# Kernel optimization log

Hardware: AMD Instinct MI355X
Metric: run time of the kernel (lower is better)

The kernel has to match this reference:

```python
import jax, jax.numpy as jnp
import numpy as np

N_GRAPHS = 256      # graphs in the batch
N_PER = 52          # nodes per peptide graph (module default num_nodes=52)
IN_CH = 21          # amino-acid one-hot features
HIDDEN = 128
OUT_EG = 128
LATENT = 64
N_LAYERS = 4


def _fc_edges(n_graphs, n_per):
    """Block-diagonal fully-connected directed edges (no self loops)."""
    base = np.arange(n_per)
    r, c = np.meshgrid(base, base, indexing='ij')
    mask = r != c
    r, c = r[mask], c[mask]                       # [n_per*(n_per-1)]
    offs = (np.arange(n_graphs) * n_per)[:, None]
    row = (r[None, :] + offs).reshape(-1)
    col = (c[None, :] + offs).reshape(-1)
    return row.astype(np.int32), col.astype(np.int32)


def setup_inputs() -> dict:
    key = jax.random.key(0)
    ks = iter(jax.random.split(key, 40))

    def rn(shape, scale=0.05):
        return jax.random.normal(next(ks), shape, dtype=jnp.float32) * scale

    N = N_GRAPHS * N_PER
    row, col = _fc_edges(N_GRAPHS, N_PER)
    L, H = N_LAYERS, HIDDEN
    return {
        'x': jax.random.normal(next(ks), (N, IN_CH), dtype=jnp.float32),
        'pos': jax.random.normal(next(ks), (N, 3), dtype=jnp.float32),
        'edge_row': jnp.asarray(row),
        'edge_col': jnp.asarray(col),
        'batch': jnp.repeat(jnp.arange(N_GRAPHS, dtype=jnp.int32), N_PER),
        'emb_in_w': rn((IN_CH, H)), 'emb_in_b': jnp.zeros((H,), jnp.float32),
        'edge_w1': rn((L, 2 * H + 1, H)), 'edge_b1': jnp.zeros((L, H), jnp.float32),
        'edge_w2': rn((L, H, H)), 'edge_b2': jnp.zeros((L, H), jnp.float32),
        'node_w1': rn((L, 2 * H, H)), 'node_b1': jnp.zeros((L, H), jnp.float32),
        'node_w2': rn((L, H, H)), 'node_b2': jnp.zeros((L, H), jnp.float32),
        'coord_w1': rn((L, H, H)), 'coord_b1': jnp.zeros((L, H), jnp.float32),
        'coord_w2': rn((L, H, 1), scale=0.001),   # xavier gain=0.001, no bias
        'emb_out_w': rn((H, OUT_EG)), 'emb_out_b': jnp.zeros((OUT_EG,), jnp.float32),
        'mean_w': rn((OUT_EG, LATENT)), 'mean_b': jnp.zeros((LATENT,), jnp.float32),
        'logvar_w': rn((OUT_EG, LATENT)), 'logvar_b': jnp.zeros((LATENT,), jnp.float32),
    }


def _segment_mean(data, ids, n):
    s = jax.ops.segment_sum(data, ids, num_segments=n)
    cnt = jax.ops.segment_sum(jnp.ones((data.shape[0],), data.dtype), ids, num_segments=n)
    return s / jnp.clip(cnt, 1.0)[:, None]


def _egcl(h, coord, row, col, p):
    """One E_GCL layer (residual=True, coords_agg='mean', no attention/tanh/normalize)."""
    ew1, eb1, ew2, eb2, nw1, nb1, nw2, nb2, cw1, cb1, cw2 = p
    n = h.shape[0]
    coord_diff = coord[row] - coord[col]                     # [E,3]
    radial = jnp.sum(coord_diff * coord_diff, axis=1, keepdims=True)  # [E,1]
    # edge model
    m = jnp.concatenate([h[row], h[col], radial], axis=1)    # [E,2H+1]
    m = jax.nn.silu(m @ ew1 + eb1)
    edge_feat = jax.nn.silu(m @ ew2 + eb2)                   # [E,H]
    # coord model: per-edge scalar, mean-aggregated onto source nodes
    t = jax.nn.silu(edge_feat @ cw1 + cb1) @ cw2             # [E,1]
    coord = coord + _segment_mean(coord_diff * t, row, n)
    # node model: sum-aggregate edge features, MLP, residual
    agg = jax.ops.segment_sum(edge_feat, row, num_segments=n)
    z = jnp.concatenate([h, agg], axis=1)                    # [N,2H]
    z = jax.nn.silu(z @ nw1 + nb1)
    h = h + (z @ nw2 + nb2)
    return h, coord


def reference(x, pos, edge_row, edge_col, batch,
              emb_in_w, emb_in_b,
              edge_w1, edge_b1, edge_w2, edge_b2,
              node_w1, node_b1, node_w2, node_b2,
              coord_w1, coord_b1, coord_w2,
              emb_out_w, emb_out_b,
              mean_w, mean_b, logvar_w, logvar_b):
    h = x @ emb_in_w + emb_in_b
    coord = pos
    for i in range(edge_w1.shape[0]):
        h, coord = _egcl(h, coord, edge_row, edge_col,
                         (edge_w1[i], edge_b1[i], edge_w2[i], edge_b2[i],
                          node_w1[i], node_b1[i], node_w2[i], node_b2[i],
                          coord_w1[i], coord_b1[i], coord_w2[i]))
    h = h @ emb_out_w + emb_out_b                            # embedding_out
    g = _segment_mean(h, batch, N_GRAPHS)                    # global_mean_pool
    mean = g @ mean_w + mean_b
    log_var = g @ logvar_w + logvar_b
    return mean, log_var
```

## Files before the change

kernel.cpp:

```cpp
#include <hip/hip_runtime.h>

constexpr int NPER = 52;
constexpr int HID  = 128;
constexpr int INCH = 21;
constexpr int NLAY = 4;
constexpr int LATD = 64;
constexpr int NGRAPH = 256;
constexpr int TPB  = 1024;
constexpr int TSTR = 424;
constexpr int TILE = 16 * TSTR;

typedef short short8 __attribute__((ext_vector_type(8)));
typedef float f32x4  __attribute__((ext_vector_type(4)));

constexpr int W1T_OFF = 0;
constexpr int W1T_SZ  = NLAY * 256 * HID;
constexpr int W2T_OFF = W1T_OFF + W1T_SZ;
constexpr int W2T_SZ  = NLAY * HID * HID;
constexpr int C1T_OFF = W2T_OFF + W2T_SZ;
constexpr int C1T_SZ  = NLAY * HID * HID;
constexpr int N1T_OFF = C1T_OFF + C1T_SZ;
constexpr int N1T_SZ  = NLAY * HID * 2 * HID;
constexpr int N2T_OFF = N1T_OFF + N1T_SZ;
constexpr int N2T_SZ  = NLAY * HID * HID;
constexpr int WS_ELEMS = N2T_OFF + N2T_SZ;

__device__ __forceinline__ unsigned cvt_pk_bf16(float a, float b) {
    unsigned r;
    asm("v_cvt_pk_bf16_f32 %0, %1, %2" : "=v"(r) : "v"(a), "v"(b));
    return r;
}
__device__ __forceinline__ unsigned short f2bf(float f) {
    return (unsigned short)cvt_pk_bf16(f, f);
}
__device__ __forceinline__ float bf2f(unsigned short h) {
    return __uint_as_float(((unsigned)h) << 16);
}
__device__ __forceinline__ float fast_rcp(float x) {
    float r;
    asm("v_rcp_f32 %0, %1" : "=v"(r) : "v"(x));
    return r;
}
__device__ __forceinline__ float silu_f(float v) {
    return v * fast_rcp(1.0f + __expf(-v));
}
__device__ __forceinline__ f32x4 mfma16(short8 a, short8 b, f32x4 c) {
    return __builtin_amdgcn_mfma_f32_16x16x32_bf16(a, b, c, 0, 0, 0);
}

__device__ __forceinline__ int tidx(int row, int e) {
    return (e >> 3) * TSTR + row * 8 + (e & 7);
}

__global__ void conv_w(const float* __restrict__ ew1, const float* __restrict__ ew2,
                       const float* __restrict__ cw1, const float* __restrict__ nw1,
                       const float* __restrict__ nw2, unsigned short* __restrict__ ws)
{
    int idx = blockIdx.x * 256 + threadIdx.x;
    if (idx >= WS_ELEMS) return;
    float v;
    if (idx < W2T_OFF) {
        int t = idx - W1T_OFF;
        int L = t / (256 * HID), rem = t % (256 * HID);
        int n = rem / HID, k = rem % HID;
        v = (n < HID) ? ew1[(size_t)L * 257 * HID + k * HID + n]
                      : ew1[(size_t)L * 257 * HID + (HID + k) * HID + (n - HID)];
    } else if (idx < C1T_OFF) {
        int t = idx - W2T_OFF;
        int L = t / (HID * HID), rem = t % (HID * HID);
        int n = rem / HID, k = rem % HID;
        v = ew2[(size_t)L * HID * HID + k * HID + n];
    } else if (idx < N1T_OFF) {
        int t = idx - C1T_OFF;
        int L = t / (HID * HID), rem = t % (HID * HID);
        int n = rem / HID, k = rem % HID;
        v = cw1[(size_t)L * HID * HID + k * HID + n];
    } else if (idx < N2T_OFF) {
        int t = idx - N1T_OFF;
        int L = t / (HID * 2 * HID), rem = t % (HID * 2 * HID);
        int n = rem / (2 * HID), k = rem % (2 * HID);
        v = nw1[(size_t)L * 2 * HID * HID + k * HID + n];
    } else {
        int t = idx - N2T_OFF;
        int L = t / (HID * HID), rem = t % (HID * HID);
        int n = rem / HID, k = rem % HID;
        v = nw2[(size_t)L * HID * HID + k * HID + n];
    }
    ws[idx] = f2bf(v);
}

constexpr int LDS_FLOATS = 1024 + 156 + 156 + 128 + 512 + 128;
constexpr size_t SHMEM_BYTES = (size_t)8 * TILE * 2 + LDS_FLOATS * 4;

__device__ __forceinline__ void coord_agg(int r, int rr, const float* tpart,
                                          const float* coord_s, float* cacc_s, int lane)
{
    float dx = 0.f, dy = 0.f, dz = 0.f;
    if (lane < NPER) {
        const float* tb = tpart + rr * 256;
        float tc = tb[lane] + tb[64 + lane] + tb[128 + lane] + tb[192 + lane];
        dx = (coord_s[r * 3 + 0] - coord_s[lane * 3 + 0]) * tc;
        dy = (coord_s[r * 3 + 1] - coord_s[lane * 3 + 1]) * tc;
        dz = (coord_s[r * 3 + 2] - coord_s[lane * 3 + 2]) * tc;
    }
    #pragma unroll
    for (int m = 1; m < 64; m <<= 1) {
        dx += __shfl_xor(dx, m); dy += __shfl_xor(dy, m); dz += __shfl_xor(dz, m);
    }
    if (lane == 0) {
        cacc_s[r * 3 + 0] = dx; cacc_s[r * 3 + 1] = dy; cacc_s[r * 3 + 2] = dz;
    }
}

extern "C" __global__ void __launch_bounds__(TPB)
egnn_mfma(const float* __restrict__ x, const float* __restrict__ pos,
          const float* __restrict__ emb_in_w, const float* __restrict__ emb_in_b,
          const float* __restrict__ edge_w1,
          const float* __restrict__ edge_b1, const float* __restrict__ edge_b2,
          const float* __restrict__ node_b1, const float* __restrict__ node_b2,
          const float* __restrict__ coord_b1, const float* __restrict__ coord_w2,
          const float* __restrict__ emb_out_w, const float* __restrict__ emb_out_b,
          const float* __restrict__ mean_w, const float* __restrict__ mean_b,
          const float* __restrict__ logvar_w, const float* __restrict__ logvar_b,
          const unsigned short* __restrict__ ws, float* __restrict__ out)
{
    extern __shared__ __align__(16) char smem[];
    unsigned short* m0_t = (unsigned short*)smem;
    unsigned short* m1_t = m0_t + TILE;
    unsigned short* e0_t = m1_t + TILE;
    unsigned short* e1_t = e0_t + TILE;
    unsigned short* h_t  = e1_t + TILE;
    unsigned short* ag_t = h_t  + TILE;
    unsigned short* A_t  = ag_t + TILE;
    unsigned short* B_t  = A_t  + TILE;
    float* aggp    = (float*)(B_t + TILE);
    float* coord_s = aggp + 1024;
    float* cacc_s  = coord_s + 156;
    float* rad_s   = cacc_s + 156;
    float* tpart   = rad_s + 128;
    float* wr_s    = tpart + 512;

    const int g    = blockIdx.x;
    const int tid  = threadIdx.x;
    const int lane = tid & 63;
    const int wv   = tid >> 6;
    const int mp   = wv >> 2;
    const int np   = wv & 3;
    const int l15  = lane & 15;
    const int kb   = lane >> 4;
    const int rowA = mp * 16 + l15;
    const int crow0 = mp * 16 + kb * 4;
    const int n0   = 32 * np + l15;
    const int n1   = n0 + 16;
    const int jp   = 2 * lane;
    const int pb   = (jp >> 3) * TSTR + (jp & 7);
    const int fo   = kb * TSTR + rowA * 8;

    {
        float* xs = (float*)m0_t;
        for (int p = tid; p < NPER * INCH; p += TPB) xs[p] = x[(size_t)g * NPER * INCH + p];
        for (int p = tid; p < NPER * 3; p += TPB)    coord_s[p] = pos[(size_t)g * NPER * 3 + p];
    }
    __syncthreads();

    for (int p = tid; p < NPER * HID; p += TPB) {
        int c = p >> 7, j = p & 127;
        float s = emb_in_b[j];
        #pragma unroll 7
        for (int k = 0; k < INCH; ++k) s += ((float*)m0_t)[c * INCH + k] * emb_in_w[k * HID + j];
        h_t[tidx(c, j)] = f2bf(s);
    }
    __syncthreads();

    for (int L = 0; L < NLAY; ++L) {
        const unsigned short* w1t = ws + W1T_OFF + (size_t)L * 256 * HID;
        const unsigned short* w2t = ws + W2T_OFF + (size_t)L * HID * HID;
        const unsigned short* c1t = ws + C1T_OFF + (size_t)L * HID * HID;
        const unsigned short* n1t = ws + N1T_OFF + (size_t)L * HID * 2 * HID;
        const unsigned short* n2t = ws + N2T_OFF + (size_t)L * HID * HID;

        short8 wE[8], wC[8];
        #pragma unroll
        for (int s = 0; s < 4; ++s) {
            wE[s]     = *(const short8*)(w2t + (size_t)n0 * HID + 32 * s + 8 * kb);
            wE[4 + s] = *(const short8*)(w2t + (size_t)n1 * HID + 32 * s + 8 * kb);
            wC[s]     = *(const short8*)(c1t + (size_t)n0 * HID + 32 * s + 8 * kb);
            wC[4 + s] = *(const short8*)(c1t + (size_t)n1 * HID + 32 * s + 8 * kb);
        }
        float eb2v[2], cb1v[2], cw2v[2];
        eb2v[0] = edge_b2[L * HID + n0];  eb2v[1] = edge_b2[L * HID + n1];
        cb1v[0] = coord_b1[L * HID + n0]; cb1v[1] = coord_b1[L * HID + n1];
        cw2v[0] = coord_w2[L * HID + n0]; cw2v[1] = coord_w2[L * HID + n1];
        if (tid < HID) wr_s[tid] = edge_w1[(size_t)L * 257 * HID + 256 * HID + tid];

        {
            f32x4 acc[4];
            #pragma unroll
            for (int q = 0; q < 4; ++q) acc[q] = (f32x4){0.f, 0.f, 0.f, 0.f};
            #pragma unroll
            for (int s = 0; s < 4; ++s) {
                short8 af = *(const short8*)(h_t + fo + s * 4 * TSTR);
                #pragma unroll
                for (int q = 0; q < 4; ++q) {
                    int n = l15 + 16 * (4 * np + q);
                    short8 bf = *(const short8*)(w1t + (size_t)n * HID + 32 * s + 8 * kb);
                    acc[q] = mfma16(af, bf, acc[q]);
                }
            }
            #pragma unroll
            for (int q = 0; q < 4; ++q) {
                int n = l15 + 16 * (4 * np + q);
                float eb1 = (n < HID) ? edge_b1[L * HID + n] : 0.f;
                #pragma unroll
                for (int reg = 0; reg < 4; ++reg) {
                    int c = crow0 + reg;
                    if (c < NPER) {
                        float v = acc[q][reg] + eb1;
                        if (n < HID) A_t[tidx(c, n)] = f2bf(v);
                        else         B_t[tidx(c, n - HID)] = f2bf(v);
                    }
                }
            }
        }
        if (tid < NPER) {
            float dx = coord_s[0] - coord_s[tid * 3 + 0];
            float dy = coord_s[1] - coord_s[tid * 3 + 1];
            float dz = coord_s[2] - coord_s[tid * 3 + 2];
            rad_s[tid] = dx * dx + dy * dy + dz * dz;
        } else if (tid >= 64 && tid < 64 + NPER) {
            int c = tid - 64;
            float dx = coord_s[3] - coord_s[c * 3 + 0];
            float dy = coord_s[4] - coord_s[c * 3 + 1];
            float dz = coord_s[5] - coord_s[c * 3 + 2];
            rad_s[64 + c] = dx * dx + dy * dy + dz * dz;
        }
        __syncthreads();

        const float wrl = wr_s[jp], wrh = wr_s[jp + 1];

        for (int gp = 0; gp < 26; ++gp) {
            const int r0 = 2 * gp, r1 = r0 + 1;

            {
                unsigned pa0 = *(const unsigned*)(A_t + pb + r0 * 8);
                unsigned pa1 = *(const unsigned*)(A_t + pb + r1 * 8);
                float A0l = bf2f((unsigned short)(pa0 & 0xffff)), A0h = bf2f((unsigned short)(pa0 >> 16));
                float A1l = bf2f((unsigned short)(pa1 & 0xffff)), A1h = bf2f((unsigned short)(pa1 >> 16));
                for (int j = wv; j < 2 * NPER; j += 16) {
                    int rr = (j >= NPER);
                    int c  = rr ? j - NPER : j;
                    float Al = rr ? A1l : A0l, Ah = rr ? A1h : A0h;
                    float rad = rad_s[rr * 64 + c];
                    unsigned bp = *(const unsigned*)(B_t + pb + c * 8);
                    float v0 = Al + bf2f((unsigned short)(bp & 0xffff)) + rad * wrl;
                    float v1 = Ah + bf2f((unsigned short)(bp >> 16))    + rad * wrh;
                    unsigned mv = cvt_pk_bf16(silu_f(v0), silu_f(v1));
                    *(unsigned*)((rr ? m1_t : m0_t) + pb + c * 8) = mv;
                }
            }
            __syncthreads();

            {
                f32x4 e00 = (f32x4){0.f,0.f,0.f,0.f}, e01 = e00, e10 = e00, e11 = e00;
                #pragma unroll
                for (int s = 0; s < 4; ++s) {
                    short8 af0 = *(const short8*)(m0_t + fo + s * 4 * TSTR);
                    short8 af1 = *(const short8*)(m1_t + fo + s * 4 * TSTR);
                    e00 = mfma16(af0, wE[s], e00); e01 = mfma16(af0, wE[4 + s], e01);
                    e10 = mfma16(af1, wE[s], e10); e11 = mfma16(af1, wE[4 + s], e11);
                }
                #pragma unroll
                for (int rr = 0; rr < 2; ++rr) {
                    f32x4 ea = rr ? e10 : e00, eb = rr ? e11 : e01;
                    unsigned short* et = rr ? e1_t : e0_t;
                    const int r = rr ? r1 : r0;
                    float a0 = 0.f, a1 = 0.f;
                    #pragma unroll
                    for (int reg = 0; reg < 4; ++reg) {
                        int c = crow0 + reg;
                        float v0 = silu_f(ea[reg] + eb2v[0]);
                        float v1 = silu_f(eb[reg] + eb2v[1]);
                        if (c < NPER) {
                            et[tidx(c, n0)] = f2bf(v0);
                            et[tidx(c, n1)] = f2bf(v1);
                            if (c != r) { a0 += v0; a1 += v1; }
                        }
                    }
                    a0 += __shfl_xor(a0, 16); a0 += __shfl_xor(a0, 32);
                    a1 += __shfl_xor(a1, 16); a1 += __shfl_xor(a1, 32);
                    if (kb == 0) {
                        float* ar = aggp + (rr * 4 + mp) * HID;
                        ar[n0] = a0; ar[n1] = a1;
                    }
                }
                if (wv < 2 && gp > 0) coord_agg(2 * gp - 2 + wv, wv, tpart, coord_s, cacc_s, lane);
            }
            __syncthreads();

            {
                f32x4 y00 = (f32x4){0.f,0.f,0.f,0.f}, y01 = y00, y10 = y00, y11 = y00;
                #pragma unroll
                for (int s = 0; s < 4; ++s) {
                    short8 af0 = *(const short8*)(e0_t + fo + s * 4 * TSTR);
                    short8 af1 = *(const short8*)(e1_t + fo + s * 4 * TSTR);
                    y00 = mfma16(af0, wC[s], y00); y01 = mfma16(af0, wC[4 + s], y01);
                    y10 = mfma16(af1, wC[s], y10); y11 = mfma16(af1, wC[4 + s], y11);
                }
                #pragma unroll
                for (int rr = 0; rr < 2; ++rr) {
                    f32x4 ya = rr ? y10 : y00, yb = rr ? y11 : y01;
                    float* tp = tpart + (rr * 4 + np) * 64;
                    #pragma unroll
                    for (int reg = 0; reg < 4; ++reg) {
                        float v = silu_f(ya[reg] + cb1v[0]) * cw2v[0]
                                + silu_f(yb[reg] + cb1v[1]) * cw2v[1];
                        v += __shfl_xor(v, 1); v += __shfl_xor(v, 2);
                        v += __shfl_xor(v, 4); v += __shfl_xor(v, 8);
                        if (l15 == 0) tp[crow0 + reg] = v;
                    }
                }
            }
            if (tid < 256) {
                int rr = tid >> 7, t = tid & 127;
                const float* ap = aggp + rr * 512;
                float a = ap[t] + ap[128 + t] + ap[256 + t] + ap[384 + t];
                ag_t[tidx(2 * gp + rr, t)] = f2bf(a);
            } else if (tid < 384 && gp + 1 < 26) {
                int t = tid - 256, rr = t >> 6, c = t & 63;
                if (c < NPER) {
                    int r = 2 * (gp + 1) + rr;
                    float dx = coord_s[r * 3 + 0] - coord_s[c * 3 + 0];
                    float dy = coord_s[r * 3 + 1] - coord_s[c * 3 + 1];
                    float dz = coord_s[r * 3 + 2] - coord_s[c * 3 + 2];
                    rad_s[rr * 64 + c] = dx * dx + dy * dy + dz * dz;
                }
            }
            __syncthreads();
        }

        if (wv < 2) coord_agg(50 + wv, wv, tpart, coord_s, cacc_s, lane);
        {
            float nb1v[2];
            nb1v[0] = node_b1[L * HID + n0]; nb1v[1] = node_b1[L * HID + n1];
            f32x4 z0 = (f32x4){0.f,0.f,0.f,0.f}, z1 = z0;
            #pragma unroll
            for (int s = 0; s < 4; ++s) {
                short8 af = *(const short8*)(h_t + fo + s * 4 * TSTR);
                z0 = mfma16(af, *(const short8*)(n1t + (size_t)n0 * 2 * HID + 32 * s + 8 * kb), z0);
                z1 = mfma16(af, *(const short8*)(n1t + (size_t)n1 * 2 * HID + 32 * s + 8 * kb), z1);
            }
            #pragma unroll
            for (int s = 0; s < 4; ++s) {
                short8 af = *(const short8*)(ag_t + fo + s * 4 * TSTR);
                z0 = mfma16(af, *(const short8*)(n1t + (size_t)n0 * 2 * HID + HID + 32 * s + 8 * kb), z0);
                z1 = mfma16(af, *(const short8*)(n1t + (size_t)n1 * 2 * HID + HID + 32 * s + 8 * kb), z1);
            }
            #pragma unroll
            for (int reg = 0; reg < 4; ++reg) {
                int c = crow0 + reg;
                if (c < NPER) {
                    m0_t[tidx(c, n0)] = f2bf(silu_f(z0[reg] + nb1v[0]));
                    m0_t[tidx(c, n1)] = f2bf(silu_f(z1[reg] + nb1v[1]));
                }
            }
        }
        __syncthreads();

        if (tid < NPER * 3) coord_s[tid] += cacc_s[tid] * (1.0f / 51.0f);
        {
            float nb2v[2];
            nb2v[0] = node_b2[L * HID + n0]; nb2v[1] = node_b2[L * HID + n1];
            f32x4 d0 = (f32x4){0.f,0.f,0.f,0.f}, d1 = d0;
            #pragma unroll
            for (int s = 0; s < 4; ++s) {
                short8 af = *(const short8*)(m0_t + fo + s * 4 * TSTR);
                d0 = mfma16(af, *(const short8*)(n2t + (size_t)n0 * HID + 32 * s + 8 * kb), d0);
                d1 = mfma16(af, *(const short8*)(n2t + (size_t)n1 * HID + 32 * s + 8 * kb), d1);
            }
            #pragma unroll
            for (int reg = 0; reg < 4; ++reg) {
                int c = crow0 + reg;
                if (c < NPER) {
                    int i0 = tidx(c, n0), i1 = tidx(c, n1);
                    h_t[i0] = f2bf(bf2f(h_t[i0]) + d0[reg] + nb2v[0]);
                    h_t[i1] = f2bf(bf2f(h_t[i1]) + d1[reg] + nb2v[1]);
                }
            }
        }
        __syncthreads();
    }

    float* gm = aggp;
    float* eg = aggp + HID;
    if (tid < HID) {
        float s = 0.f;
        for (int c = 0; c < NPER; ++c) s += bf2f(h_t[tidx(c, tid)]);
        gm[tid] = s * (1.0f / 52.0f);
    }
    __syncthreads();
    if (tid < HID) {
        float s = emb_out_b[tid];
        #pragma unroll 4
        for (int k = 0; k < HID; ++k) s += gm[k] * emb_out_w[k * HID + tid];
        eg[tid] = s;
    }
    __syncthreads();
    if (tid < 2 * LATD) {
        const int  l   = tid & (LATD - 1);
        const bool ism = tid < LATD;
        const float* W = ism ? mean_w : logvar_w;
        float s = ism ? mean_b[l] : logvar_b[l];
        #pragma unroll 4
        for (int k = 0; k < HID; ++k) s += eg[k] * W[k * LATD + l];
        out[(ism ? 0 : NGRAPH * LATD) + g * LATD + l] = s;
    }
}

extern "C" void kernel_launch(void* const* d_in, const int* in_sizes, int n_in,
                              void* d_out, int out_size, void* d_ws, size_t ws_size,
                              hipStream_t stream) {
    const float* x         = (const float*)d_in[0];
    const float* pos       = (const float*)d_in[1];
    const float* emb_in_w  = (const float*)d_in[5];
    const float* emb_in_b  = (const float*)d_in[6];
    const float* edge_w1   = (const float*)d_in[7];
    const float* edge_b1   = (const float*)d_in[8];
    const float* edge_w2   = (const float*)d_in[9];
    const float* edge_b2   = (const float*)d_in[10];
    const float* node_w1   = (const float*)d_in[11];
    const float* node_b1   = (const float*)d_in[12];
    const float* node_w2   = (const float*)d_in[13];
    const float* node_b2   = (const float*)d_in[14];
    const float* coord_w1  = (const float*)d_in[15];
    const float* coord_b1  = (const float*)d_in[16];
    const float* coord_w2  = (const float*)d_in[17];
    const float* emb_out_w = (const float*)d_in[18];
    const float* emb_out_b = (const float*)d_in[19];
    const float* mean_w    = (const float*)d_in[20];
    const float* mean_b    = (const float*)d_in[21];
    const float* logvar_w  = (const float*)d_in[22];
    const float* logvar_b  = (const float*)d_in[23];

    unsigned short* ws = (unsigned short*)d_ws;

    conv_w<<<(WS_ELEMS + 255) / 256, 256, 0, stream>>>(edge_w1, edge_w2, coord_w1,
                                                       node_w1, node_w2, ws);

    (void)hipFuncSetAttribute(reinterpret_cast<const void*>(egnn_mfma),
                              hipFuncAttributeMaxDynamicSharedMemorySize,
                              (int)SHMEM_BYTES);

    hipLaunchKernelGGL(egnn_mfma, dim3(NGRAPH), dim3(TPB), SHMEM_BYTES, stream,
                       x, pos, emb_in_w, emb_in_b, edge_w1,
                       edge_b1, edge_b2, node_b1, node_b2,
                       coord_b1, coord_w2, emb_out_w, emb_out_b,
                       mean_w, mean_b, logvar_w, logvar_b,
                       ws, (float*)d_out);
}
```

Baseline: 805.7 us.

## Warp-specialize edge loop: producer waves build messages while consumer waves run MFMAs

The per-pair edge loop is split by role. Waves 0-7 compute the next row pair's SiLU edge inputs with vectorized 4-wide loads from row-major A/B buffers. Waves 8-15 run the edge and coord MLP MFMAs on the current pair, covering 32 rows each, using double-buffered message tiles. Coordinate aggregation, radial precompute and agg reduction are folded into the producer side, which removes one barrier per iteration, but only half the waves now issue MFMAs.

After: 1.444 ms. +79.3%, slower.

```diff
diff --git a/kernel.cpp b/kernel.cpp
--- a/kernel.cpp
+++ b/kernel.cpp
@@ -36,6 +36,8 @@
 __device__ __forceinline__ float bf2f(unsigned short h) {
     return __uint_as_float(((unsigned)h) << 16);
 }
+__device__ __forceinline__ float blo(unsigned u) { return __uint_as_float(u << 16); }
+__device__ __forceinline__ float bhi(unsigned u) { return __uint_as_float(u & 0xffff0000u); }
 __device__ __forceinline__ float fast_rcp(float x) {
     float r;
     asm("v_rcp_f32 %0, %1" : "=v"(r) : "v"(x));
@@ -47,7 +49,6 @@
 __device__ __forceinline__ f32x4 mfma16(short8 a, short8 b, f32x4 c) {
     return __builtin_amdgcn_mfma_f32_16x16x32_bf16(a, b, c, 0, 0, 0);
 }
-
 __device__ __forceinline__ int tidx(int row, int e) {
     return (e >> 3) * TSTR + row * 8 + (e & 7);
 }
@@ -89,28 +90,9 @@
     ws[idx] = f2bf(v);
 }
 
-constexpr int LDS_FLOATS = 1024 + 156 + 156 + 128 + 512 + 128;
-constexpr size_t SHMEM_BYTES = (size_t)8 * TILE * 2 + LDS_FLOATS * 4;
-
-__device__ __forceinline__ void coord_agg(int r, int rr, const float* tpart,
-                                          const float* coord_s, float* cacc_s, int lane)
-{
-    float dx = 0.f, dy = 0.f, dz = 0.f;
-    if (lane < NPER) {
-        const float* tb = tpart + rr * 256;
-        float tc = tb[lane] + tb[64 + lane] + tb[128 + lane] + tb[192 + lane];
-        dx = (coord_s[r * 3 + 0] - coord_s[lane * 3 + 0]) * tc;
-        dy = (coord_s[r * 3 + 1] - coord_s[lane * 3 + 1]) * tc;
-        dz = (coord_s[r * 3 + 2] - coord_s[lane * 3 + 2]) * tc;
-    }
-    #pragma unroll
-    for (int m = 1; m < 64; m <<= 1) {
-        dx += __shfl_xor(dx, m); dy += __shfl_xor(dy, m); dz += __shfl_xor(dz, m);
-    }
-    if (lane == 0) {
-        cacc_s[r * 3 + 0] = dx; cacc_s[r * 3 + 1] = dy; cacc_s[r * 3 + 2] = dz;
-    }
-}
+constexpr int LDS_SHORTS = 8 * TILE + 2 * NPER * HID;
+constexpr int LDS_FLOATS = 128 + 256 + 1024 + 512 + 156 + 156;
+constexpr size_t SHMEM_BYTES = (size_t)LDS_SHORTS * 2 + (size_t)LDS_FLOATS * 4;
 
 extern "C" __global__ void __launch_bounds__(TPB)
 egnn_mfma(const float* __restrict__ x, const float* __restrict__ pos,
@@ -125,39 +107,49 @@
           const unsigned short* __restrict__ ws, float* __restrict__ out)
 {
     extern __shared__ __align__(16) char smem[];
-    unsigned short* m0_t = (unsigned short*)smem;
-    unsigned short* m1_t = m0_t + TILE;
-    unsigned short* e0_t = m1_t + TILE;
-    unsigned short* e1_t = e0_t + TILE;
-    unsigned short* h_t  = e1_t + TILE;
-    unsigned short* ag_t = h_t  + TILE;
-    unsigned short* A_t  = ag_t + TILE;
-    unsigned short* B_t  = A_t  + TILE;
-    float* aggp    = (float*)(B_t + TILE);
-    float* coord_s = aggp + 1024;
+    unsigned short* mb   = (unsigned short*)smem;
+    unsigned short* ef_t = mb + 4 * TILE;
+    unsigned short* h_t  = ef_t + 2 * TILE;
+    unsigned short* ag_t = h_t + TILE;
+    unsigned short* A_l  = ag_t + TILE;
+    unsigned short* B_l  = A_l + NPER * HID;
+    float* wr_s   = (float*)(B_l + NPER * HID);
+    float* rad_s  = wr_s + 128;
+    float* tpartp = rad_s + 256;
+    float* aggf   = tpartp + 1024;
+    float* coord_s = aggf + 512;
     float* cacc_s  = coord_s + 156;
-    float* rad_s   = cacc_s + 156;
-    float* tpart   = rad_s + 128;
-    float* wr_s    = tpart + 512;
 
     const int g    = blockIdx.x;
     const int tid  = threadIdx.x;
     const int lane = tid & 63;
     const int wv   = tid >> 6;
-    const int mp   = wv >> 2;
-    const int np   = wv & 3;
     const int l15  = lane & 15;
     const int kb   = lane >> 4;
-    const int rowA = mp * 16 + l15;
-    const int crow0 = mp * 16 + kb * 4;
-    const int n0   = 32 * np + l15;
-    const int n1   = n0 + 16;
-    const int jp   = 2 * lane;
-    const int pb   = (jp >> 3) * TSTR + (jp & 7);
-    const int fo   = kb * TSTR + rowA * 8;
+    const bool cons = (wv >= 8);
+
+    const int mp4 = wv >> 2, np4 = wv & 3;
+    const int rowA4 = mp4 * 16 + l15;
+    const int crow4 = mp4 * 16 + kb * 4;
+    const int n0_4 = 32 * np4 + l15, n1_4 = n0_4 + 16;
+
+    const int mpc = (wv >> 2) & 1;
+    const int npc = wv & 3;
+    const int rw0 = mpc * 32 + l15, rw1 = rw0 + 16;
+    const int rowc = mpc * 32 + kb * 4;
+    const int nc0 = npc * 32 + l15, nc1 = nc0 + 16;
+    const int eb0 = (nc0 >> 3) * TSTR + (nc0 & 7);
+    const int eb1x = (nc1 >> 3) * TSTR + (nc1 & 7);
+
+    const int pw = wv;
+    const int rrp = pw >> 2;
+    const int cb = 13 * pw - 52 * rrp;
+    const int half = lane >> 5;
+    const int col4 = (lane & 31) * 4;
+    const int wb = (col4 >> 3) * TSTR + (col4 & 7);
 
     {
-        float* xs = (float*)m0_t;
+        float* xs = (float*)mb;
         for (int p = tid; p < NPER * INCH; p += TPB) xs[p] = x[(size_t)g * NPER * INCH + p];
         for (int p = tid; p < NPER * 3; p += TPB)    coord_s[p] = pos[(size_t)g * NPER * 3 + p];
     }
@@ -167,7 +159,7 @@
         int c = p >> 7, j = p & 127;
         float s = emb_in_b[j];
         #pragma unroll 7
-        for (int k = 0; k < INCH; ++k) s += ((float*)m0_t)[c * INCH + k] * emb_in_w[k * HID + j];
+        for (int k = 0; k < INCH; ++k) s += ((float*)mb)[c * INCH + k] * emb_in_w[k * HID + j];
         h_t[tidx(c, j)] = f2bf(s);
     }
     __syncthreads();
@@ -179,209 +171,290 @@
         const unsigned short* n1t = ws + N1T_OFF + (size_t)L * HID * 2 * HID;
         const unsigned short* n2t = ws + N2T_OFF + (size_t)L * HID * HID;
 
-        short8 wE[8], wC[8];
-        #pragma unroll
-        for (int s = 0; s < 4; ++s) {
-            wE[s]     = *(const short8*)(w2t + (size_t)n0 * HID + 32 * s + 8 * kb);
-            wE[4 + s] = *(const short8*)(w2t + (size_t)n1 * HID + 32 * s + 8 * kb);
-            wC[s]     = *(const short8*)(c1t + (size_t)n0 * HID + 32 * s + 8 * kb);
-            wC[4 + s] = *(const short8*)(c1t + (size_t)n1 * HID + 32 * s + 8 * kb);
-        }
-        float eb2v[2], cb1v[2], cw2v[2];
-        eb2v[0] = edge_b2[L * HID + n0];  eb2v[1] = edge_b2[L * HID + n1];
-        cb1v[0] = coord_b1[L * HID + n0]; cb1v[1] = coord_b1[L * HID + n1];
-        cw2v[0] = coord_w2[L * HID + n0]; cw2v[1] = coord_w2[L * HID + n1];
-        if (tid < HID) wr_s[tid] = edge_w1[(size_t)L * 257 * HID + 256 * HID + tid];
-
         {
             f32x4 acc[4];
             #pragma unroll
             for (int q = 0; q < 4; ++q) acc[q] = (f32x4){0.f, 0.f, 0.f, 0.f};
             #pragma unroll
             for (int s = 0; s < 4; ++s) {
-                short8 af = *(const short8*)(h_t + fo + s * 4 * TSTR);
+                short8 af = *(const short8*)(h_t + (4 * s + kb) * TSTR + rowA4 * 8);
                 #pragma unroll
                 for (int q = 0; q < 4; ++q) {
-                    int n = l15 + 16 * (4 * np + q);
+                    int n = l15 + 16 * (4 * np4 + q);
                     short8 bf = *(const short8*)(w1t + (size_t)n * HID + 32 * s + 8 * kb);
                     acc[q] = mfma16(af, bf, acc[q]);
                 }
             }
             #pragma unroll
             for (int q = 0; q < 4; ++q) {
-                int n = l15 + 16 * (4 * np + q);
+                int n = l15 + 16 * (4 * np4 + q);
                 float eb1 = (n < HID) ? edge_b1[L * HID + n] : 0.f;
                 #pragma unroll
                 for (int reg = 0; reg < 4; ++reg) {
-                    int c = crow0 + reg;
+                    int c = crow4 + reg;
                     if (c < NPER) {
                         float v = acc[q][reg] + eb1;
-                        if (n < HID) A_t[tidx(c, n)] = f2bf(v);
-                        else         B_t[tidx(c, n - HID)] = f2bf(v);
-                    }
-                }
-            }
-        }
-        if (tid < NPER) {
-            float dx = coord_s[0] - coord_s[tid * 3 + 0];
-            float dy = coord_s[1] - coord_s[tid * 3 + 1];
-            float dz = coord_s[2] - coord_s[tid * 3 + 2];
-            rad_s[tid] = dx * dx + dy * dy + dz * dz;
-        } else if (tid >= 64 && tid < 64 + NPER) {
-            int c = tid - 64;
-            float dx = coord_s[3] - coord_s[c * 3 + 0];
-            float dy = coord_s[4] - coord_s[c * 3 + 1];
-            float dz = coord_s[5] - coord_s[c * 3 + 2];
-            rad_s[64 + c] = dx * dx + dy * dy + dz * dz;
+                        if (n < HID) A_l[c * HID + n] = f2bf(v);
+                        else         B_l[c * HID + (n - HID)] = f2bf(v);
+                    }
+                }
+            }
+            if (tid < HID) wr_s[tid] = edge_w1[(size_t)L * 257 * HID + 256 * HID + tid];
+            if (wv < 4 && lane < NPER) {
+                int r = wv;
+                float dx = coord_s[r * 3 + 0] - coord_s[lane * 3 + 0];
+                float dy = coord_s[r * 3 + 1] - coord_s[lane * 3 + 1];
+                float dz = coord_s[r * 3 + 2] - coord_s[lane * 3 + 2];
+                rad_s[(r >> 1) * 128 + (r & 1) * 64 + lane] = dx * dx + dy * dy + dz * dz;
+            }
         }
         __syncthreads();
 
-        const float wrl = wr_s[jp], wrh = wr_s[jp + 1];
-
-        for (int gp = 0; gp < 26; ++gp) {
-            const int r0 = 2 * gp, r1 = r0 + 1;
-
-            {
-                unsigned pa0 = *(const unsigned*)(A_t + pb + r0 * 8);
-                unsigned pa1 = *(const unsigned*)(A_t + pb + r1 * 8);
-                float A0l = bf2f((unsigned short)(pa0 & 0xffff)), A0h = bf2f((unsigned short)(pa0 >> 16));
-                float A1l = bf2f((unsigned short)(pa1 & 0xffff)), A1h = bf2f((unsigned short)(pa1 >> 16));
-                for (int j = wv; j < 2 * NPER; j += 16) {
-                    int rr = (j >= NPER);
-                    int c  = rr ? j - NPER : j;
-                    float Al = rr ? A1l : A0l, Ah = rr ? A1h : A0h;
-                    float rad = rad_s[rr * 64 + c];
-                    unsigned bp = *(const unsigned*)(B_t + pb + c * 8);
-                    float v0 = Al + bf2f((unsigned short)(bp & 0xffff)) + rad * wrl;
-                    float v1 = Ah + bf2f((unsigned short)(bp >> 16))    + rad * wrh;
-                    unsigned mv = cvt_pk_bf16(silu_f(v0), silu_f(v1));
-                    *(unsigned*)((rr ? m1_t : m0_t) + pb + c * 8) = mv;
-                }
-            }
-            __syncthreads();
-
-            {
-                f32x4 e00 = (f32x4){0.f,0.f,0.f,0.f}, e01 = e00, e10 = e00, e11 = e00;
-                #pragma unroll
-                for (int s = 0; s < 4; ++s) {
-                    short8 af0 = *(const short8*)(m0_t + fo + s * 4 * TSTR);
-                    short8 af1 = *(const short8*)(m1_t + fo + s * 4 * TSTR);
-                    e00 = mfma16(af0, wE[s], e00); e01 = mfma16(af0, wE[4 + s], e01);
-                    e10 = mfma16(af1, wE[s], e10); e11 = mfma16(af1, wE[4 + s], e11);
-                }
+        short8 wE0[4], wE1[4], wC0[4], wC1[4];
+        float eb2v[2], cb1v[2], cw2v[2];
+
+        if (cons) {
+            #pragma unroll
+            for (int s = 0; s < 4; ++s) {
+                wE0[s] = *(const short8*)(w2t + (size_t)nc0 * HID + 32 * s + 8 * kb);
+                wE1[s] = *(const short8*)(w2t + (size_t)nc1 * HID + 32 * s + 8 * kb);
+                wC0[s] = *(const short8*)(c1t + (size_t)nc0 * HID + 32 * s + 8 * kb);
+                wC1[s] = *(const short8*)(c1t + (size_t)nc1 * HID + 32 * s + 8 * kb);
+            }
+            eb2v[0] = edge_b2[L * HID + nc0];  eb2v[1] = edge_b2[L * HID + nc1];
+            cb1v[0] = coord_b1[L * HID + nc0]; cb1v[1] = coord_b1[L * HID + nc1];
+            cw2v[0] = coord_w2[L * HID + nc0]; cw2v[1] = coord_w2[L * HID + nc1];
+        } else {
+            const int pt = 0;
+            const int r = 2 * pt + rrp;
+            unsigned short* mt_ = mb + ((pt & 1) * 2 + rrp) * TILE;
+            const float* radp = rad_s + (pt & 1) * 128 + rrp * 64;
+            uint2 a2 = *(const uint2*)(A_l + r * HID + col4);
+            float A0 = blo(a2.x), A1 = bhi(a2.x), A2 = blo(a2.y), A3 = bhi(a2.y);
+            float4 w4 = *(const float4*)(wr_s + col4);
+            #pragma unroll
+            for (int i = 0; i < 7; ++i) {
+                int lr = 2 * i + half;
+                if (lr < 13) {
+                    int c = cb + lr;
+                    float rad = radp[c];
+                    uint2 b2 = *(const uint2*)(B_l + c * HID + col4);
+                    float v0 = A0 + blo(b2.x) + rad * w4.x;
+                    float v1 = A1 + bhi(b2.x) + rad * w4.y;
+                    float v2 = A2 + blo(b2.y) + rad * w4.z;
+                    float v3 = A3 + bhi(b2.y) + rad * w4.w;
+                    uint2 o;
+                    o.x = cvt_pk_bf16(silu_f(v0), silu_f(v1));
+                    o.y = cvt_pk_bf16(silu_f(v2), silu_f(v3));
+                    *(uint2*)(mt_ + wb + c * 8) = o;
+                }
+            }
+        }
+        __syncthreads();
+
+        for (int p = 0; p < 26; ++p) {
+            if (cons) {
                 #pragma unroll
                 for (int rr = 0; rr < 2; ++rr) {
-                    f32x4 ea = rr ? e10 : e00, eb = rr ? e11 : e01;
-                    unsigned short* et = rr ? e1_t : e0_t;
-                    const int r = rr ? r1 : r0;
-                    float a0 = 0.f, a1 = 0.f;
+                    const unsigned short* mt_ = mb + ((p & 1) * 2 + rr) * TILE;
+                    f32x4 a00 = (f32x4){0.f,0.f,0.f,0.f}, a01 = a00, a10 = a00, a11 = a00;
                     #pragma unroll
-                    for (int reg = 0; reg < 4; ++reg) {
-                        int c = crow0 + reg;
-                        float v0 = silu_f(ea[reg] + eb2v[0]);
-                        float v1 = silu_f(eb[reg] + eb2v[1]);
-                        if (c < NPER) {
-                            et[tidx(c, n0)] = f2bf(v0);
-                            et[tidx(c, n1)] = f2bf(v1);
-                            if (c != r) { a0 += v0; a1 += v1; }
+                    for (int s = 0; s < 4; ++s) {
+                        short8 f0 = *(const short8*)(mt_ + (4 * s + kb) * TSTR + rw0 * 8);
+                        short8 f1 = *(const short8*)(mt_ + (4 * s + kb) * TSTR + rw1 * 8);
+                        a00 = mfma16(f0, wE0[s], a00);
+                        a01 = mfma16(f0, wE1[s], a01);
+                        a10 = mfma16(f1, wE0[s], a10);
+                        a11 = mfma16(f1, wE1[s], a11);
+                    }
+                    const int r = 2 * p + rr;
+                    unsigned short* et = ef_t + rr * TILE;
+                    float as0 = 0.f, as1 = 0.f;
+                    #pragma unroll
+                    for (int mt2 = 0; mt2 < 2; ++mt2) {
+                        f32x4 va = mt2 ? a10 : a00;
+                        f32x4 vb = mt2 ? a11 : a01;
+                        #pragma unroll
+                        for (int reg = 0; reg < 4; ++reg) {
+                            int c = rowc + mt2 * 16 + reg;
+                            float v0 = silu_f(va[reg] + eb2v[0]);
+                            float v1 = silu_f(vb[reg] + eb2v[1]);
+                            if (c < NPER) {
+                                et[eb0 + c * 8] = f2bf(v0);
+                                et[eb1x + c * 8] = f2bf(v1);
+                                if (c != r) { as0 += v0; as1 += v1; }
+                            }
                         }
                     }
-                    a0 += __shfl_xor(a0, 16); a0 += __shfl_xor(a0, 32);
-                    a1 += __shfl_xor(a1, 16); a1 += __shfl_xor(a1, 32);
+                    as0 += __shfl_xor(as0, 16); as0 += __shfl_xor(as0, 32);
+                    as1 += __shfl_xor(as1, 16); as1 += __shfl_xor(as1, 32);
                     if (kb == 0) {
-                        float* ar = aggp + (rr * 4 + mp) * HID;
-                        ar[n0] = a0; ar[n1] = a1;
-                    }
-                }
-                if (wv < 2 && gp > 0) coord_agg(2 * gp - 2 + wv, wv, tpart, coord_s, cacc_s, lane);
+                        aggf[(mpc * 2 + rr) * HID + nc0] = as0;
+                        aggf[(mpc * 2 + rr) * HID + nc1] = as1;
+                    }
+                }
+            } else if (p + 1 < 26) {
+                const int pt = p + 1;
+                const int r = 2 * pt + rrp;
+                unsigned short* mt_ = mb + ((pt & 1) * 2 + rrp) * TILE;
+                const float* radp = rad_s + (pt & 1) * 128 + rrp * 64;
+                uint2 a2 = *(const uint2*)(A_l + r * HID + col4);
+                float A0 = blo(a2.x), A1 = bhi(a2.x), A2 = blo(a2.y), A3 = bhi(a2.y);
+                float4 w4 = *(const float4*)(wr_s + col4);
+                #pragma unroll
+                for (int i = 0; i < 7; ++i) {
+                    int lr = 2 * i + half;
+                    if (lr < 13) {
+                        int c = cb + lr;
+                        float rad = radp[c];
+                        uint2 b2 = *(const uint2*)(B_l + c * HID + col4);
+                        float v0 = A0 + blo(b2.x) + rad * w4.x;
+                        float v1 = A1 + bhi(b2.x) + rad * w4.y;
+                        float v2 = A2 + blo(b2.y) + rad * w4.z;
+                        float v3 = A3 + bhi(b2.y) + rad * w4.w;
+                        uint2 o;
+                        o.x = cvt_pk_bf16(silu_f(v0), silu_f(v1));
+                        o.y = cvt_pk_bf16(silu_f(v2), silu_f(v3));
+                        *(uint2*)(mt_ + wb + c * 8) = o;
+                    }
+                }
             }
             __syncthreads();
 
-            {
-                f32x4 y00 = (f32x4){0.f,0.f,0.f,0.f}, y01 = y00, y10 = y00, y11 = y00;
-                #pragma unroll
-                for (int s = 0; s < 4; ++s) {
-                    short8 af0 = *(const short8*)(e0_t + fo + s * 4 * TSTR);
-                    short8 af1 = *(const short8*)(e1_t + fo + s * 4 * TSTR);
-                    y00 = mfma16(af0, wC[s], y00); y01 = mfma16(af0, wC[4 + s], y01);
-                    y10 = mfma16(af1, wC[s], y10); y11 = mfma16(af1, wC[4 + s], y11);
-                }
+            if (cons) {
                 #pragma unroll
                 for (int rr = 0; rr < 2; ++rr) {
-                    f32x4 ya = rr ? y10 : y00, yb = rr ? y11 : y01;
-                    float* tp = tpart + (rr * 4 + np) * 64;
+                    const unsigned short* et = ef_t + rr * TILE;
+                    f32x4 a00 = (f32x4){0.f,0.f,0.f,0.f}, a01 = a00, a10 = a00, a11 = a00;
                     #pragma unroll
-                    for (int reg = 0; reg < 4; ++reg) {
-                        float v = silu_f(ya[reg] + cb1v[0]) * cw2v[0]
-                                + silu_f(yb[reg] + cb1v[1]) * cw2v[1];
-                        v += __shfl_xor(v, 1); v += __shfl_xor(v, 2);
-                        v += __shfl_xor(v, 4); v += __shfl_xor(v, 8);
-                        if (l15 == 0) tp[crow0 + reg] = v;
-                    }
-                }
-            }
-            if (tid < 256) {
-                int rr = tid >> 7, t = tid & 127;
-                const float* ap = aggp + rr * 512;
-                float a = ap[t] + ap[128 + t] + ap[256 + t] + ap[384 + t];
-                ag_t[tidx(2 * gp + rr, t)] = f2bf(a);
-            } else if (tid < 384 && gp + 1 < 26) {
-                int t = tid - 256, rr = t >> 6, c = t & 63;
-                if (c < NPER) {
-                    int r = 2 * (gp + 1) + rr;
-                    float dx = coord_s[r * 3 + 0] - coord_s[c * 3 + 0];
-                    float dy = coord_s[r * 3 + 1] - coord_s[c * 3 + 1];
-                    float dz = coord_s[r * 3 + 2] - coord_s[c * 3 + 2];
-                    rad_s[rr * 64 + c] = dx * dx + dy * dy + dz * dz;
+                    for (int s = 0; s < 4; ++s) {
+                        short8 f0 = *(const short8*)(et + (4 * s + kb) * TSTR + rw0 * 8);
+                        short8 f1 = *(const short8*)(et + (4 * s + kb) * TSTR + rw1 * 8);
+                        a00 = mfma16(f0, wC0[s], a00);
+                        a01 = mfma16(f0, wC1[s], a01);
+                        a10 = mfma16(f1, wC0[s], a10);
+                        a11 = mfma16(f1, wC1[s], a11);
+                    }
+                    float* tpb = tpartp + ((p & 1) * 2 + rr) * 256 + npc * 64;
+                    #pragma unroll
+                    for (int mt2 = 0; mt2 < 2; ++mt2) {
+                        f32x4 va = mt2 ? a10 : a00;
+                        f32x4 vb = mt2 ? a11 : a01;
+                        #pragma unroll
+                        for (int reg = 0; reg < 4; ++reg) {
+                            float t = silu_f(va[reg] + cb1v[0]) * cw2v[0]
+                                    + silu_f(vb[reg] + cb1v[1]) * cw2v[1];
+                            t += __shfl_xor(t, 1); t += __shfl_xor(t, 2);
+                            t += __shfl_xor(t, 4); t += __shfl_xor(t, 8);
+                            if (l15 == 0) tpb[rowc + mt2 * 16 + reg] = t;
+                        }
+                    }
+                }
+            } else {
+                if (wv < 2) {
+                    if (p > 0) {
+                        const int rr = wv, r = 2 * (p - 1) + rr;
+                        const float* tb = tpartp + (((p - 1) & 1) * 2 + rr) * 256;
+                        float dx = 0.f, dy = 0.f, dz = 0.f;
+                        if (lane < NPER) {
+                            float tc = tb[lane] + tb[64 + lane] + tb[128 + lane] + tb[192 + lane];
+                            dx = (coord_s[r * 3 + 0] - coord_s[lane * 3 + 0]) * tc;
+                            dy = (coord_s[r * 3 + 1] - coord_s[lane * 3 + 1]) * tc;
+                            dz = (coord_s[r * 3 + 2] - coord_s[lane * 3 + 2]) * tc;
+                        }
+                        #pragma unroll
+                        for (int m = 1; m < 64; m <<= 1) {
+                            dx += __shfl_xor(dx, m); dy += __shfl_xor(dy, m); dz += __shfl_xor(dz, m);
+                        }
+                        if (lane == 0) {
+                            cacc_s[r * 3 + 0] = dx; cacc_s[r * 3 + 1] = dy; cacc_s[r * 3 + 2] = dz;
+                        }
+                    }
+                } else if (wv < 4) {
+                    if (p < 24 && lane < NPER) {
+                        const int rr = wv - 2, rn = 2 * (p + 2) + rr;
+                        float dx = coord_s[rn * 3 + 0] - coord_s[lane * 3 + 0];
+                        float dy = coord_s[rn * 3 + 1] - coord_s[lane * 3 + 1];
+                        float dz = coord_s[rn * 3 + 2] - coord_s[lane * 3 + 2];
+                        rad_s[(p & 1) * 128 + rr * 64 + lane] = dx * dx + dy * dy + dz * dz;
+                    }
+                } else if (wv < 6) {
+                    const int rr = wv - 4, r = 2 * p + rr;
+                    #pragma unroll
+                    for (int hh = 0; hh < 2; ++hh) {
+                        int col = lane + hh * 64;
+                        float s = aggf[rr * HID + col] + aggf[(2 + rr) * HID + col];
+                        ag_t[(col >> 3) * TSTR + r * 8 + (col & 7)] = f2bf(s);
+                    }
                 }
             }
             __syncthreads();
         }
 
-        if (wv < 2) coord_agg(50 + wv, wv, tpart, coord_s, cacc_s, lane);
+        if (wv < 2) {
+            const int rr = wv, r = 50 + rr;
+            const float* tb = tpartp + (1 * 2 + rr) * 256;
+            float dx = 0.f, dy = 0.f, dz = 0.f;
+            if (lane < NPER) {
+                float tc = tb[lane] + tb[64 + lane] + tb[128 + lane] + tb[192 + lane];
+                dx = (coord_s[r * 3 + 0] - coord_s[lane * 3 + 0]) * tc;
+                dy = (coord_s[r * 3 + 1] - coord_s[lane * 3 + 1]) * tc;
+                dz = (coord_s[r * 3 + 2] - coord_s[lane * 3 + 2]) * tc;
+            }
+            #pragma unroll
+            for (int m = 1; m < 64; m <<= 1) {
+                dx += __shfl_xor(dx, m); dy += __shfl_xor(dy, m); dz += __shfl_xor(dz, m);
+            }
+            if (lane == 0) {
+                cacc_s[r * 3 + 0] = dx; cacc_s[r * 3 + 1] = dy; cacc_s[r * 3 + 2] = dz;
+            }
+        }
+        __syncthreads();
+
+        if (tid < NPER * 3) coord_s[tid] += cacc_s[tid] * (1.0f / 51.0f);
         {
             float nb1v[2];
-            nb1v[0] = node_b1[L * HID + n0]; nb1v[1] = node_b1[L * HID + n1];
+            nb1v[0] = node_b1[L * HID + n0_4]; nb1v[1] = node_b1[L * HID + n1_4];
             f32x4 z0 = (f32x4){0.f,0.f,0.f,0.f}, z1 = z0;
             #pragma unroll
             for (int s = 0; s < 4; ++s) {
-                short8 af = *(const short8*)(h_t + fo + s * 4 * TSTR);
-                z0 = mfma16(af, *(const short8*)(n1t + (size_t)n0 * 2 * HID + 32 * s + 8 * kb), z0);
-                z1 = mfma16(af, *(const short8*)(n1t + (size_t)n1 * 2 * HID + 32 * s + 8 * kb), z1);
+                short8 af = *(const short8*)(h_t + (4 * s + kb) * TSTR + rowA4 * 8);
+                z0 = mfma16(af, *(const short8*)(n1t + (size_t)n0_4 * 2 * HID + 32 * s + 8 * kb), z0);
+                z1 = mfma16(af, *(const short8*)(n1t + (size_t)n1_4 * 2 * HID + 32 * s + 8 * kb), z1);
             }
             #pragma unroll
             for (int s = 0; s < 4; ++s) {
-                short8 af = *(const short8*)(ag_t + fo + s * 4 * TSTR);
-                z0 = mfma16(af, *(const short8*)(n1t + (size_t)n0 * 2 * HID + HID + 32 * s + 8 * kb), z0);
-                z1 = mfma16(af, *(const short8*)(n1t + (size_t)n1 * 2 * HID + HID + 32 * s + 8 * kb), z1);
-            }
+                short8 af = *(const short8*)(ag_t + (4 * s + kb) * TSTR + rowA4 * 8);
+                z0 = mfma16(af, *(const short8*)(n1t + (size_t)n0_4 * 2 * HID + HID + 32 * s + 8 * kb), z0);
+                z1 = mfma16(af, *(const short8*)(n1t + (size_t)n1_4 * 2 * HID + HID + 32 * s + 8 * kb), z1);
+            }
+            __syncthreads();
             #pragma unroll
             for (int reg = 0; reg < 4; ++reg) {
-                int c = crow0 + reg;
+                int c = crow4 + reg;
                 if (c < NPER) {
-                    m0_t[tidx(c, n0)] = f2bf(silu_f(z0[reg] + nb1v[0]));
-                    m0_t[tidx(c, n1)] = f2bf(silu_f(z1[reg] + nb1v[1]));
+                    mb[tidx(c, n0_4)] = f2bf(silu_f(z0[reg] + nb1v[0]));
+                    mb[tidx(c, n1_4)] = f2bf(silu_f(z1[reg] + nb1v[1]));
                 }
             }
         }
         __syncthreads();
 
-        if (tid < NPER * 3) coord_s[tid] += cacc_s[tid] * (1.0f / 51.0f);
         {
             float nb2v[2];
-            nb2v[0] = node_b2[L * HID + n0]; nb2v[1] = node_b2[L * HID + n1];
+            nb2v[0] = node_b2[L * HID + n0_4]; nb2v[1] = node_b2[L * HID + n1_4];
             f32x4 d0 = (f32x4){0.f,0.f,0.f,0.f}, d1 = d0;
             #pragma unroll
             for (int s = 0; s < 4; ++s) {
-                short8 af = *(const short8*)(m0_t + fo + s * 4 * TSTR);
-                d0 = mfma16(af, *(const short8*)(n2t + (size_t)n0 * HID + 32 * s + 8 * kb), d0);
-                d1 = mfma16(af, *(const short8*)(n2t + (size_t)n1 * HID + 32 * s + 8 * kb), d1);
+                short8 af = *(const short8*)(mb + (4 * s + kb) * TSTR + rowA4 * 8);
+                d0 = mfma16(af, *(const short8*)(n2t + (size_t)n0_4 * HID + 32 * s + 8 * kb), d0);
+                d1 = mfma16(af, *(const short8*)(n2t + (size_t)n1_4 * HID + 32 * s + 8 * kb), d1);
             }
             #pragma unroll
             for (int reg = 0; reg < 4; ++reg) {
-                int c = crow0 + reg;
+                int c = crow4 + reg;
                 if (c < NPER) {
-                    int i0 = tidx(c, n0), i1 = tidx(c, n1);
+                    int i0 = tidx(c, n0_4), i1 = tidx(c, n1_4);
                     h_t[i0] = f2bf(bf2f(h_t[i0]) + d0[reg] + nb2v[0]);
                     h_t[i1] = f2bf(bf2f(h_t[i1]) + d1[reg] + nb2v[1]);
                 }
@@ -390,8 +463,8 @@
         __syncthreads();
     }
 
-    float* gm = aggp;
-    float* eg = aggp + HID;
+    float* gm = aggf;
+    float* eg = aggf + HID;
     if (tid < HID) {
         float s = 0.f;
         for (int c = 0; c < NPER; ++c) s += bf2f(h_t[tidx(c, tid)]);
```
